# Kernel tuning notes

Measured on AMD Instinct MI355X. Metric: run time of the kernel, lower is better.

The kernel has to match this reference:

```python
import jax, jax.numpy as jnp
import numpy as np

N_HEAD = 16
N_EMBED = 1024

def setup_inputs() -> dict:
    key = jax.random.key(0)
    ks = jax.random.split(key, 5)
    C = N_EMBED
    x = jax.random.normal(ks[0], (2, 2048, C), dtype=jnp.float32)
    # c_attn: Linear(C, 3C); c_proj: Linear(C, C). PyTorch Linear: y = x @ W.T + b
    w_attn = jax.random.normal(ks[1], (3 * C, C), dtype=jnp.float32) * (1.0 / np.sqrt(C))
    b_attn = jnp.zeros((3 * C,), dtype=jnp.float32)
    w_proj = jax.random.normal(ks[2], (C, C), dtype=jnp.float32) * (1.0 / np.sqrt(C))
    b_proj = jnp.zeros((C,), dtype=jnp.float32)
    return {"x": x, "w_attn": w_attn, "b_attn": b_attn, "w_proj": w_proj, "b_proj": b_proj}

def reference(x, w_attn, b_attn, w_proj, b_proj):
    B, T, C = x.shape
    H = N_HEAD
    D = C // H
    qkv = jnp.einsum('btc,fc->btf', x, w_attn) + b_attn  # [B,T,3C]
    q, k, v = jnp.split(qkv, 3, axis=-1)
    # [B,H,T,D]
    q = q.reshape(B, T, H, D).transpose(0, 2, 1, 3)
    k = k.reshape(B, T, H, D).transpose(0, 2, 1, 3)
    v = v.reshape(B, T, H, D).transpose(0, 2, 1, 3)
    att = jnp.einsum('bhqd,bhkd->bhqk', q, k) * (1.0 / np.sqrt(D))  # [B,H,T,T]
    causal = jnp.tril(jnp.ones((T, T), dtype=bool))
    att = jnp.where(causal[None, None], att, jnp.finfo(att.dtype).min)
    att = jax.nn.softmax(att, axis=-1)
    y = jnp.einsum('bhqk,bhkd->bhqd', att, v)  # [B,H,T,D]
    y = y.transpose(0, 2, 1, 3).reshape(B, T, C)
    return jnp.einsum('btc,fc->btf', y, w_proj) + b_proj
```

## Files before the change

### kernel.cpp

```cpp
#include <hip/hip_runtime.h>
#include <hip/hip_bf16.h>

typedef unsigned short u16;
typedef __attribute__((ext_vector_type(8))) short v8s;
typedef __attribute__((ext_vector_type(4))) short v4s;
typedef __attribute__((ext_vector_type(4))) float v4f;

#define SCL2 0.180336879f

__device__ __forceinline__ u16 f2bu(float f) {
  union { float f; unsigned u; } v; v.f = f;
  unsigned r = (v.u + 0x7fffu + ((v.u >> 16) & 1u)) >> 16;
  return (u16)r;
}
__device__ __forceinline__ v4s pack4(const v4f& a) {
  union { v4s s; __hip_bfloat162 h[2]; } u;
  u.h[0] = __float22bfloat162_rn(make_float2(a[0], a[1]));
  u.h[1] = __float22bfloat162_rn(make_float2(a[2], a[3]));
  return u.s;
}
__device__ __forceinline__ v8s pack8(const v4f& a, const v4f& b) {
  union { v8s s; __hip_bfloat162 h[4]; } u;
  u.h[0] = __float22bfloat162_rn(make_float2(a[0], a[1]));
  u.h[1] = __float22bfloat162_rn(make_float2(a[2], a[3]));
  u.h[2] = __float22bfloat162_rn(make_float2(b[0], b[1]));
  u.h[3] = __float22bfloat162_rn(make_float2(b[2], b[3]));
  return u.s;
}

__device__ __forceinline__ void g2l16(const u16* g, u16* l) {
  __builtin_amdgcn_global_load_lds((const __attribute__((address_space(1))) void*)g,
                                   (__attribute__((address_space(3))) void*)l,
                                   16, 0, 0);
}

__global__ __launch_bounds__(256) void cvt_bf16(const float* __restrict__ s0, u16* __restrict__ d0, int n0,
                                                const float* __restrict__ s1, u16* __restrict__ d1, int n1,
                                                const float* __restrict__ s2, u16* __restrict__ d2, int n2) {
  int total8 = (n0 + n1 + n2) >> 3;
  for (int i = blockIdx.x * blockDim.x + threadIdx.x; i < total8; i += gridDim.x * blockDim.x) {
    int e = i << 3;
    const float* s; u16* d;
    if (e < n0)            { s = s0 + e;            d = d0 + e; }
    else if (e < n0 + n1)  { s = s1 + (e - n0);     d = d1 + (e - n0); }
    else                   { s = s2 + (e - n0 - n1); d = d2 + (e - n0 - n1); }
    v4f a = *(const v4f*)s, b = *(const v4f*)(s + 4);
    *(v8s*)d = pack8(a, b);
  }
}

__global__ __launch_bounds__(256) void gemm_qkv(const u16* __restrict__ A,
                                                const u16* __restrict__ W,
                                                const float* __restrict__ bias,
                                                u16* __restrict__ o0,
                                                u16* __restrict__ o1,
                                                u16* __restrict__ o2) {
  constexpr int K = 1024;
  __shared__ __align__(16) u16 As[128 * 64];
  __shared__ __align__(16) u16 Bs[128 * 64];
  const int tid = threadIdx.x;
  const int w = tid >> 6, lane = tid & 63, l15 = lane & 15, quad = lane >> 4;
  const int wm = w & 1, wn = w >> 1;
  const int R0 = blockIdx.x * 128, C0 = blockIdx.y * 128;

  v4f acc[4][4] = {};
  const u16* Ag = A + (size_t)R0 * K;
  const u16* Wg = W + (size_t)C0 * K;

  int srow[4], scol[4], sdst[4];
#pragma unroll
  for (int i = 0; i < 4; ++i) {
    int p = (w * 4 + i) * 64 + lane;
    srow[i] = p >> 3;
    scol[i] = (p & 7) * 8;
    sdst[i] = (w * 4 + i) * 512;
  }

  for (int k0 = 0; k0 < K; k0 += 64) {
    if (k0) __syncthreads();
#pragma unroll
    for (int i = 0; i < 4; ++i) g2l16(Ag + srow[i] * K + k0 + scol[i], &As[sdst[i]]);
#pragma unroll
    for (int i = 0; i < 4; ++i) g2l16(Wg + srow[i] * K + k0 + scol[i], &Bs[sdst[i]]);
    __syncthreads();
#pragma unroll
    for (int kk = 0; kk < 2; ++kk) {
      v8s a[4], b[4];
#pragma unroll
      for (int m = 0; m < 4; ++m)
        a[m] = *(const v8s*)&As[(wm * 64 + m * 16 + l15) * 64 + (kk * 4 + quad) * 8];
#pragma unroll
      for (int n = 0; n < 4; ++n)
        b[n] = *(const v8s*)&Bs[(wn * 64 + n * 16 + l15) * 64 + (kk * 4 + quad) * 8];
#pragma unroll
      for (int m = 0; m < 4; ++m)
#pragma unroll
        for (int n = 0; n < 4; ++n)
          acc[m][n] = __builtin_amdgcn_mfma_f32_16x16x32_bf16(a[m], b[n], acc[m][n], 0, 0, 0);
    }
  }

#pragma unroll
  for (int n = 0; n < 4; ++n) {
    int f = C0 + wn * 64 + n * 16 + l15;
    float bv = bias[f];
#pragma unroll
    for (int m = 0; m < 4; ++m) {
      int r0 = R0 + wm * 64 + m * 16 + quad * 4;
      int which = f >> 10, c = f & 1023;
      int h = c >> 6, d = c & 63;
      int b = r0 >> 11, t = r0 & 2047;
      if (which == 2) {
        v4s pk;
#pragma unroll
        for (int reg = 0; reg < 4; ++reg) pk[reg] = (short)f2bu(acc[m][n][reg] + bv);
        *(v4s*)&o2[(((b << 4) + h) * 64 + d) * 2048 + t] = pk;
      } else {
        u16* dst = (which == 0) ? o0 : o1;
        float sc = (which == 0) ? SCL2 : 1.0f;
#pragma unroll
        for (int reg = 0; reg < 4; ++reg)
          dst[(((b << 4) + h) * 2048 + (t + reg)) * 64 + d] = f2bu((acc[m][n][reg] + bv) * sc);
      }
    }
  }
}

__global__ __launch_bounds__(256) void gemm_proj(const u16* __restrict__ A,
                                                 const u16* __restrict__ W,
                                                 const float* __restrict__ bias,
                                                 float* __restrict__ out) {
  constexpr int K = 1024;
  __shared__ __align__(16) u16 As[128 * 64];
  __shared__ __align__(16) u16 Bs[64 * 64];
  const int tid = threadIdx.x;
  const int w = tid >> 6, lane = tid & 63, l15 = lane & 15, quad = lane >> 4;
  const int wm = w & 1, wn = w >> 1;
  const int R0 = blockIdx.x * 128, C0 = blockIdx.y * 64;

  v4f acc[4][2] = {};
  const u16* Ag = A + (size_t)R0 * K;
  const u16* Wg = W + (size_t)C0 * K;

  int arow[4], acol[4], adst[4];
#pragma unroll
  for (int i = 0; i < 4; ++i) {
    int p = (w * 4 + i) * 64 + lane;
    arow[i] = p >> 3; acol[i] = (p & 7) * 8; adst[i] = (w * 4 + i) * 512;
  }
  int brow[2], bcol[2], bdst[2];
#pragma unroll
  for (int i = 0; i < 2; ++i) {
    int p = (w * 2 + i) * 64 + lane;
    brow[i] = p >> 3; bcol[i] = (p & 7) * 8; bdst[i] = (w * 2 + i) * 512;
  }

  for (int k0 = 0; k0 < K; k0 += 64) {
    if (k0) __syncthreads();
#pragma unroll
    for (int i = 0; i < 4; ++i) g2l16(Ag + arow[i] * K + k0 + acol[i], &As[adst[i]]);
#pragma unroll
    for (int i = 0; i < 2; ++i) g2l16(Wg + brow[i] * K + k0 + bcol[i], &Bs[bdst[i]]);
    __syncthreads();
#pragma unroll
    for (int kk = 0; kk < 2; ++kk) {
      v8s a[4], b[2];
#pragma unroll
      for (int m = 0; m < 4; ++m)
        a[m] = *(const v8s*)&As[(wm * 64 + m * 16 + l15) * 64 + (kk * 4 + quad) * 8];
#pragma unroll
      for (int n = 0; n < 2; ++n)
        b[n] = *(const v8s*)&Bs[(wn * 32 + n * 16 + l15) * 64 + (kk * 4 + quad) * 8];
#pragma unroll
      for (int m = 0; m < 4; ++m)
#pragma unroll
        for (int n = 0; n < 2; ++n)
          acc[m][n] = __builtin_amdgcn_mfma_f32_16x16x32_bf16(a[m], b[n], acc[m][n], 0, 0, 0);
    }
  }

#pragma unroll
  for (int n = 0; n < 2; ++n) {
    int f = C0 + wn * 32 + n * 16 + l15;
    float bv = bias[f];
#pragma unroll
    for (int m = 0; m < 4; ++m) {
      int r0 = R0 + wm * 64 + m * 16 + quad * 4;
#pragma unroll
      for (int reg = 0; reg < 4; ++reg)
        out[(size_t)(r0 + reg) * 1024 + f] = acc[m][n][reg] + bv;
    }
  }
}

__global__ __launch_bounds__(512, 4) void attn_kernel(const u16* __restrict__ Q,
                                                      const u16* __restrict__ Kt,
                                                      const u16* __restrict__ Vt,
                                                      u16* __restrict__ Y) {
  __shared__ __align__(16) u16 Ksh[2][64 * 64], Vsh[2][64 * 64];
  __shared__ __align__(16) u16 Psh[8 * 16 * 72];
  const int tid = threadIdx.x;
  const int w = tid >> 6, lane = tid & 63, l15 = lane & 15, quad = lane >> 4;
  const int pi = blockIdx.x, h = blockIdx.y, b = blockIdx.z;
  const int myqt = (w < 4) ? pi : 31 - pi;
  const int strip = w & 3;
  const int q0 = myqt * 64 + strip * 16;
  const int KT = 32 - pi;
  const int bh = b * 16 + h;
  const u16* qg = Q + bh * 131072;
  const u16* kg = Kt + bh * 131072;
  const u16* vg = Vt + bh * 131072;

  v8s aq[2];
  {
    const u16* qr = qg + (q0 + l15) * 64;
    aq[0] = *(const v8s*)(qr + quad * 8);
    aq[1] = *(const v8s*)(qr + 32 + quad * 8);
  }

  v4f O[4] = {};
  float ll = 0.f;
  const int rowlim = strip * 16 + l15;

  const int srow = tid >> 3, cc = tid & 7;
  const int sgc = cc * 8, ssc = (cc ^ (srow & 7)) * 8;
  v8s tk = *(const v8s*)(kg + srow * 64 + sgc);
  v8s tv = *(const v8s*)(vg + srow * 2048 + sgc);

  u16* Pw = &Psh[w * 16 * 72];

  for (int kt = 0; kt < KT; ++kt) {
    const int buf = kt & 1;
    *(v8s*)&Ksh[buf][srow * 64 + ssc] = tk;
    *(v8s*)&Vsh[buf][srow * 64 + ssc] = tv;
    __syncthreads();
    if (kt + 1 < KT) {
      int kn = (kt + 1) * 64;
      tk = *(const v8s*)(kg + (kn + srow) * 64 + sgc);
      tv = *(const v8s*)(vg + srow * 2048 + kn + sgc);
    }
    if (kt <= myqt) {
      const u16* Kb = Ksh[buf];
      const u16* Vb = Vsh[buf];

      v4f s[4];
#pragma unroll
      for (int nt = 0; nt < 4; ++nt) {
        v4f z = {0.f, 0.f, 0.f, 0.f};
#pragma unroll
        for (int kk = 0; kk < 2; ++kk) {
          v8s kf = *(const v8s*)&Kb[(nt * 16 + l15) * 64 + (((kk * 4 + quad) ^ (l15 & 7)) * 8)];
          z = __builtin_amdgcn_mfma_f32_16x16x32_bf16(kf, aq[kk], z, 0, 0, 0);
        }
        s[nt] = z;
      }

      float rs = 0.f;
      if (kt == myqt) {
#pragma unroll
        for (int nt = 0; nt < 4; ++nt)
#pragma unroll
          for (int reg = 0; reg < 4; ++reg) {
            int kl = nt * 16 + quad * 4 + reg;
            float p = (kl <= rowlim) ? exp2f(s[nt][reg]) : 0.f;
            s[nt][reg] = p; rs += p;
          }
      } else {
#pragma unroll
        for (int nt = 0; nt < 4; ++nt)
#pragma unroll
          for (int reg = 0; reg < 4; ++reg) {
            float p = exp2f(s[nt][reg]);
            s[nt][reg] = p; rs += p;
          }
      }
      ll += rs;
#pragma unroll
      for (int nt = 0; nt < 4; ++nt)
        *(v4s*)&Pw[l15 * 72 + nt * 16 + quad * 4] = pack4(s[nt]);

      asm volatile("" ::: "memory");
      v8s ap[2];
      ap[0] = *(const v8s*)&Pw[l15 * 72 + quad * 8];
      ap[1] = *(const v8s*)&Pw[l15 * 72 + 32 + quad * 8];
#pragma unroll
      for (int nt = 0; nt < 4; ++nt)
#pragma unroll
        for (int kk = 0; kk < 2; ++kk) {
          v8s vf = *(const v8s*)&Vb[(nt * 16 + l15) * 64 + (((kk * 4 + quad) ^ (l15 & 7)) * 8)];
          O[nt] = __builtin_amdgcn_mfma_f32_16x16x32_bf16(ap[kk], vf, O[nt], 0, 0, 0);
        }
    }
  }

  ll += __shfl_xor(ll, 16, 64); ll += __shfl_xor(ll, 32, 64);
  float li = 1.f / ll, lO[4];
#pragma unroll
  for (int reg = 0; reg < 4; ++reg) lO[reg] = __shfl(li, quad * 4 + reg, 64);
  const int tb = q0 + quad * 4;
#pragma unroll
  for (int nt = 0; nt < 4; ++nt)
#pragma unroll
    for (int reg = 0; reg < 4; ++reg)
      Y[(b * 2048 + tb + reg) * 1024 + h * 64 + nt * 16 + l15] = f2bu(O[nt][reg] * lO[reg]);
}

extern "C" void kernel_launch(void* const* d_in, const int* in_sizes, int n_in,
                              void* d_out, int out_size, void* d_ws, size_t ws_size,
                              hipStream_t stream) {
  const float* x      = (const float*)d_in[0];
  const float* w_attn = (const float*)d_in[1];
  const float* b_attn = (const float*)d_in[2];
  const float* w_proj = (const float*)d_in[3];
  const float* b_proj = (const float*)d_in[4];
  float* out = (float*)d_out;
  char* ws = (char*)d_ws;
  u16* xb  = (u16*)(ws);
  u16* wab = (u16*)(ws + (size_t)( 8u << 20));
  u16* wpb = (u16*)(ws + (size_t)(14u << 20));
  u16* q   = (u16*)(ws + (size_t)(16u << 20));
  u16* k   = (u16*)(ws + (size_t)(24u << 20));
  u16* vt  = (u16*)(ws + (size_t)(32u << 20));
  u16* y   = (u16*)(ws + (size_t)(40u << 20));

  cvt_bf16<<<2048, 256, 0, stream>>>(x, xb, 4194304, w_attn, wab, 3145728, w_proj, wpb, 1048576);
  gemm_qkv<<<dim3(32, 24), 256, 0, stream>>>(xb, wab, b_attn, q, k, vt);
  attn_kernel<<<dim3(16, 16, 2), 512, 0, stream>>>(q, k, vt, y);
  gemm_proj<<<dim3(32, 16), 256, 0, stream>>>(y, wpb, b_proj, out);
}
```

Before: 174.1 us.

## Redistribute P fragments in registers with permlane32 swap instead of LDS round-trip

```diff
diff --git a/kernel.cpp b/kernel.cpp
--- a/kernel.cpp
+++ b/kernel.cpp
@@ -12,12 +12,6 @@
   union { float f; unsigned u; } v; v.f = f;
   unsigned r = (v.u + 0x7fffu + ((v.u >> 16) & 1u)) >> 16;
   return (u16)r;
-}
-__device__ __forceinline__ v4s pack4(const v4f& a) {
-  union { v4s s; __hip_bfloat162 h[2]; } u;
-  u.h[0] = __float22bfloat162_rn(make_float2(a[0], a[1]));
-  u.h[1] = __float22bfloat162_rn(make_float2(a[2], a[3]));
-  return u.s;
 }
 __device__ __forceinline__ v8s pack8(const v4f& a, const v4f& b) {
   union { v8s s; __hip_bfloat162 h[4]; } u;
@@ -198,7 +192,6 @@
                                                       const u16* __restrict__ Vt,
                                                       u16* __restrict__ Y) {
   __shared__ __align__(16) u16 Ksh[2][64 * 64], Vsh[2][64 * 64];
-  __shared__ __align__(16) u16 Psh[8 * 16 * 72];
   const int tid = threadIdx.x;
   const int w = tid >> 6, lane = tid & 63, l15 = lane & 15, quad = lane >> 4;
   const int pi = blockIdx.x, h = blockIdx.y, b = blockIdx.z;
@@ -224,15 +217,20 @@
 
   const int srow = tid >> 3, cc = tid & 7;
   const int sgc = cc * 8, ssc = (cc ^ (srow & 7)) * 8;
+  const int vhi = cc >> 1, vlo = cc & 1;
+  const int vs0 = srow * 64 + (((vhi * 2)     ^ (srow & 7)) * 8) + vlo * 4;
+  const int vs1 = srow * 64 + (((vhi * 2 + 1) ^ (srow & 7)) * 8) + vlo * 4;
   v8s tk = *(const v8s*)(kg + srow * 64 + sgc);
   v8s tv = *(const v8s*)(vg + srow * 2048 + sgc);
-
-  u16* Pw = &Psh[w * 16 * 72];
 
   for (int kt = 0; kt < KT; ++kt) {
     const int buf = kt & 1;
     *(v8s*)&Ksh[buf][srow * 64 + ssc] = tk;
-    *(v8s*)&Vsh[buf][srow * 64 + ssc] = tv;
+    {
+      union { v8s v; v4s h[2]; } tvu; tvu.v = tv;
+      *(v4s*)&Vsh[buf][vs0] = tvu.h[0];
+      *(v4s*)&Vsh[buf][vs1] = tvu.h[1];
+    }
     __syncthreads();
     if (kt + 1 < KT) {
       int kn = (kt + 1) * 64;
@@ -275,14 +273,27 @@
           }
       }
       ll += rs;
-#pragma unroll
-      for (int nt = 0; nt < 4; ++nt)
-        *(v4s*)&Pw[l15 * 72 + nt * 16 + quad * 4] = pack4(s[nt]);
-
-      asm volatile("" ::: "memory");
+
+      unsigned pk0[4], pk1[4];
+#pragma unroll
+      for (int nt = 0; nt < 4; ++nt) {
+        union { __hip_bfloat162 h; unsigned u; } c0, c1;
+        c0.h = __float22bfloat162_rn(make_float2(s[nt][0], s[nt][1]));
+        c1.h = __float22bfloat162_rn(make_float2(s[nt][2], s[nt][3]));
+        pk0[nt] = c0.u; pk1[nt] = c1.u;
+      }
+      asm volatile("v_permlane32_swap_b32 %0, %1" : "+v"(pk0[0]), "+v"(pk0[1]));
+      asm volatile("v_permlane32_swap_b32 %0, %1" : "+v"(pk1[0]), "+v"(pk1[1]));
+      asm volatile("v_permlane32_swap_b32 %0, %1" : "+v"(pk0[2]), "+v"(pk0[3]));
+      asm volatile("v_permlane32_swap_b32 %0, %1" : "+v"(pk1[2]), "+v"(pk1[3]));
       v8s ap[2];
-      ap[0] = *(const v8s*)&Pw[l15 * 72 + quad * 8];
-      ap[1] = *(const v8s*)&Pw[l15 * 72 + 32 + quad * 8];
+      {
+        union { v8s v; unsigned u[4]; } a0, a1;
+        a0.u[0] = pk0[0]; a0.u[1] = pk1[0]; a0.u[2] = pk0[1]; a0.u[3] = pk1[1];
+        a1.u[0] = pk0[2]; a1.u[1] = pk1[2]; a1.u[2] = pk0[3]; a1.u[3] = pk1[3];
+        ap[0] = a0.v; ap[1] = a1.v;
+      }
+
 #pragma unroll
       for (int nt = 0; nt < 4; ++nt)
 #pragma unroll
```

After: 177.1 us. Within noise of the previous version (+1.7%).
